# Kernel optimization log

Measured on AMD Instinct MI355X. Metric: run time of the kernel, lower is better.

Reference implementation:

```python
import jax, jax.numpy as jnp
import numpy as np

VAR_EPS = 1e-5
CLAMP = 1e-7
B, S, D = 128, 1024, 256  # D = ambient Lorentz dim (time + D-1 spatial), k = 1


def linner(a, b):
    """Minkowski inner product <a,b>_L = -a0*b0 + sum_i a_i*b_i, keepdims."""
    return -a[..., :1] * b[..., :1] + jnp.sum(a[..., 1:] * b[..., 1:], axis=-1, keepdims=True)


def add_origin(x):
    # x + o where o = (1, 0, ..., 0)
    return jnp.concatenate([x[..., :1] + 1.0, x[..., 1:]], axis=-1)


def centroid(x):
    """Lorentz centroid over dim -2 (k=1): normalize the Euclidean mean back to the hyperboloid."""
    avg = jnp.mean(x, axis=-2)
    denom = jnp.sqrt(jnp.clip(jnp.abs(-linner(avg, avg)), 1e-8, None))
    return avg / denom


def logmap(x, y):
    alpha = jnp.clip(-linner(x, y), 1.0 + CLAMP, None)
    u = y - alpha * x
    return (jnp.arccosh(alpha) / jnp.sqrt(alpha * alpha - 1.0)) * u


def transp0back(x, v):
    # parallel transport from x to origin o: v - v0/(1+x0) * (x+o)
    coef = v[..., :1] / (1.0 + x[..., :1])
    return v - coef * add_origin(x)


def transp0(y, v):
    # parallel transport from origin o to y: v + <y,v>_L/(1+y0) * (o+y)
    coef = linner(y, v) / (1.0 + y[..., :1])
    return v + coef * add_origin(y)


def expmap(x, u):
    n = jnp.sqrt(jnp.clip(linner(u, u), CLAMP, None))
    return jnp.cosh(n) * x + jnp.sinh(n) * (u / n)


def expmap0_space(u_space):
    # exp map at origin from a purely-spatial tangent vector (used only for data generation)
    n = jnp.sqrt(jnp.clip(jnp.sum(u_space * u_space, axis=-1, keepdims=True), CLAMP, None))
    return jnp.concatenate([jnp.cosh(n), jnp.sinh(n) * (u_space / n)], axis=-1)


def setup_inputs() -> dict:
    key = jax.random.key(0)
    k1, = jax.random.split(key, 1)
    u_space = 0.5 * jax.random.normal(k1, (B, S, D - 1), dtype=jnp.float32)
    x = expmap0_space(u_space)  # valid points on the hyperboloid, [B,S,D]
    beta = jnp.zeros((D,), dtype=jnp.float32).at[0].set(1.0)  # manifold.origin
    gamma = jnp.ones((1,), dtype=jnp.float32)
    return {"x": x, "beta": beta, "gamma": gamma}


def reference(x, beta, gamma):
    # training-mode forward of LorentzBatchNorm_beta (3D input path)
    mean = centroid(centroid(x))            # [D] Frechet-style centroid over seq then batch
    x_t = logmap(mean, x)                   # [B,S,D] tangent at mean
    x_t = transp0back(mean, x_t)            # transport to tangent at origin
    var = jnp.sqrt(jnp.var(x_t, axis=(0, 1)) + VAR_EPS)  # [D] per-feature std
    x_t = x_t * (gamma / var)
    x_t = transp0(beta, x_t)                # transport to tangent at beta
    return expmap(beta, x_t)                # [B,S,D] back on the manifold
```

## Files before the change

kernel.cpp:

```cpp
#include <hip/hip_runtime.h>
#include <math.h>

#define BB 128
#define SS 1024
#define DD 256
#define NP (BB * SS)
#define CH 16
#define ROWS (SS / CH)
#define NB3 2048
#define NW3 (NB3 * 4)
#define RB4 32
#define NB4A (NB3 / RB4)

#define LN2F 0.69314718056f
#define L2EF 1.44269504089f
__device__ __forceinline__ float fsqrt(float x) { return __builtin_amdgcn_sqrtf(x); }
__device__ __forceinline__ float frcp(float x)  { return __builtin_amdgcn_rcpf(x); }
__device__ __forceinline__ float frsq(float x)  { return __builtin_amdgcn_rsqf(x); }
__device__ __forceinline__ float flog2(float x) { return __builtin_amdgcn_logf(x); }
__device__ __forceinline__ float fexp2(float x) { return __builtin_amdgcn_exp2f(x); }

__device__ __forceinline__ float wave_sum(float v) {
#pragma unroll
    for (int m = 32; m >= 1; m >>= 1) v += __shfl_xor(v, m, 64);
    return v;
}

__device__ __forceinline__ void wave_sum2(float& a, float& b) {
#pragma unroll
    for (int m = 32; m >= 1; m >>= 1) {
        float ta = __shfl_xor(a, m, 64);
        float tb = __shfl_xor(b, m, 64);
        a += ta;
        b += tb;
    }
}

__device__ __forceinline__ float block_sum(float v, float* red) {
    const int t = threadIdx.x;
    red[t] = v;
    __syncthreads();
#pragma unroll
    for (int off = 128; off >= 1; off >>= 1) {
        if (t < off) red[t] += red[t + off];
        __syncthreads();
    }
    float r = red[0];
    __syncthreads();
    return r;
}

__device__ __forceinline__ float dot4(float4 a, float4 b) {
    return fmaf(a.x, b.x, fmaf(a.y, b.y, fmaf(a.z, b.z, a.w * b.w)));
}

__global__ __launch_bounds__(256) void k1_partial(const float* __restrict__ x,
                                                  float* __restrict__ part) {
    const int ch = blockIdx.x, b = blockIdx.y;
    const int w = threadIdx.x >> 6, l = threadIdx.x & 63;
    const float4* x4 = (const float4*)x;
    size_t base = ((size_t)b * SS + (size_t)ch * ROWS + (size_t)w * (ROWS / 4)) * (DD / 4);
    float4 s = make_float4(0.f, 0.f, 0.f, 0.f);
#pragma unroll 4
    for (int r = 0; r < ROWS / 4; ++r) {
        float4 v = x4[base + (size_t)r * (DD / 4) + l];
        s.x += v.x; s.y += v.y; s.z += v.z; s.w += v.w;
    }
    __shared__ float lds[4][DD];
    lds[w][4 * l + 0] = s.x; lds[w][4 * l + 1] = s.y;
    lds[w][4 * l + 2] = s.z; lds[w][4 * l + 3] = s.w;
    __syncthreads();
    const int t = threadIdx.x;
    part[((size_t)b * CH + ch) * DD + t] = lds[0][t] + lds[1][t] + lds[2][t] + lds[3][t];
}

__global__ __launch_bounds__(256) void k2a_c1(const float* __restrict__ part,
                                              float* __restrict__ c1) {
    const int b = blockIdx.x;
    const int t = threadIdx.x;
    __shared__ float red[DD];
    float sx = 0.f;
#pragma unroll
    for (int ch = 0; ch < CH; ++ch) sx += part[((size_t)b * CH + ch) * DD + t];
    float avg = sx * (1.0f / SS);
    float contrib = (t == 0) ? avg * avg : -avg * avg;
    float r = block_sum(contrib, red);
    c1[(size_t)b * DD + t] = avg * frsq(fmaxf(fabsf(r), 1e-8f));
}

__global__ __launch_bounds__(256) void k2b_mean(const float* __restrict__ c1,
                                                float* __restrict__ wsmean) {
    const int t = threadIdx.x;
    __shared__ float red[DD];
    float acc = 0.f;
#pragma unroll 8
    for (int b = 0; b < BB; ++b) acc += c1[(size_t)b * DD + t];
    float avg = acc * (1.0f / BB);
    float contrib = (t == 0) ? avg * avg : -avg * avg;
    float r = block_sum(contrib, red);
    wsmean[t] = avg * frsq(fmaxf(fabsf(r), 1e-8f));
}

__device__ __forceinline__ float4 compute_xt(const float4* __restrict__ row, int l,
                                             float4 m4, float m0, float inv1pm0) {
    float4 v = row[l];
    float dp = dot4(v, m4);
    float dot = wave_sum(dp);
    float y0 = __shfl(v.x, 0, 64);
    float alpha = fmaxf(fmaf(2.0f * m0, y0, -dot), 1.0f + 1e-7f);
    float tt = fmaf(alpha, alpha, -1.0f);
    float f = (LN2F * flog2(alpha + fsqrt(tt))) * frsq(tt);
    float xt0 = f * (y0 - alpha * m0);
    float coef = xt0 * inv1pm0;
    float4 r;
    r.x = f * (v.x - alpha * m4.x) - coef * ((l == 0) ? (m0 + 1.0f) : m4.x);
    r.y = f * (v.y - alpha * m4.y) - coef * m4.y;
    r.z = f * (v.z - alpha * m4.z) - coef * m4.z;
    r.w = f * (v.w - alpha * m4.w) - coef * m4.w;
    return r;
}

__global__ __launch_bounds__(256, 8) void k3_stats(const float* __restrict__ x,
                                                   const float* __restrict__ wsmean,
                                                   float* __restrict__ part3) {
    const int w = threadIdx.x >> 6, l = threadIdx.x & 63;
    float4 m4 = ((const float4*)wsmean)[l];
    float m0 = wsmean[0];
    float inv1pm0 = frcp(1.0f + m0);
    float4 s = make_float4(0, 0, 0, 0), q = make_float4(0, 0, 0, 0);
    const int wid = blockIdx.x * 4 + w;
#pragma unroll 2
    for (int p = wid; p < NP; p += NW3) {
        const float4* row = ((const float4*)x) + (size_t)p * (DD / 4);
        float4 t4 = compute_xt(row, l, m4, m0, inv1pm0);
        s.x += t4.x; s.y += t4.y; s.z += t4.z; s.w += t4.w;
        q.x += t4.x * t4.x; q.y += t4.y * t4.y; q.z += t4.z * t4.z; q.w += t4.w * t4.w;
    }
    __shared__ float lds[4][2 * DD];
    lds[w][4 * l + 0] = s.x; lds[w][4 * l + 1] = s.y;
    lds[w][4 * l + 2] = s.z; lds[w][4 * l + 3] = s.w;
    lds[w][DD + 4 * l + 0] = q.x; lds[w][DD + 4 * l + 1] = q.y;
    lds[w][DD + 4 * l + 2] = q.z; lds[w][DD + 4 * l + 3] = q.w;
    __syncthreads();
    const int t = threadIdx.x;
    part3[(size_t)blockIdx.x * (2 * DD) + t]      = lds[0][t] + lds[1][t] + lds[2][t] + lds[3][t];
    part3[(size_t)blockIdx.x * (2 * DD) + DD + t] = lds[0][DD + t] + lds[1][DD + t] + lds[2][DD + t] + lds[3][DD + t];
}

__global__ __launch_bounds__(512) void k4a_reduce(const float* __restrict__ part3,
                                                  float* __restrict__ stage2) {
    const int t = threadIdx.x;
    const int r0 = blockIdx.x * RB4;
    float s = 0.f;
#pragma unroll 8
    for (int r = 0; r < RB4; ++r) s += part3[(size_t)(r0 + r) * (2 * DD) + t];
    stage2[(size_t)blockIdx.x * (2 * DD) + t] = s;
}

__global__ __launch_bounds__(256) void k4b_scale(const float* __restrict__ stage2,
                                                 const float* __restrict__ gamma,
                                                 float* __restrict__ wsscale) {
    const int t = threadIdx.x;
    double s1 = 0.0, s2 = 0.0;
    for (int i = 0; i < NB4A; ++i) {
        s1 += (double)stage2[(size_t)i * (2 * DD) + t];
        s2 += (double)stage2[(size_t)i * (2 * DD) + DD + t];
    }
    const double N = (double)NP;
    double mv = s1 / N;
    double var = s2 / N - mv * mv;
    wsscale[t] = gamma[0] * frsq((float)var + 1e-5f);
}

__global__ __launch_bounds__(256, 8) void k5_out(const float* __restrict__ x,
                                                 const float* __restrict__ wsmean,
                                                 const float* __restrict__ wsscale,
                                                 const float* __restrict__ beta,
                                                 float4* __restrict__ out4) {
    const int w = threadIdx.x >> 6, l = threadIdx.x & 63;
    float4 m4 = ((const float4*)wsmean)[l];
    float m0 = wsmean[0];
    float inv1pm0 = frcp(1.0f + m0);
    float4 sc = ((const float4*)wsscale)[l];
    float4 b4 = ((const float4*)beta)[l];
    float b0 = beta[0];
    float inv1pb0 = frcp(1.0f + b0);
    float b0p1 = b0 + 1.0f;
    const int wid = blockIdx.x * 4 + w;
#pragma unroll 2
    for (int p = wid; p < NP; p += NW3) {
        const float4* row = ((const float4*)x) + (size_t)p * (DD / 4);
        float4 t4 = compute_xt(row, l, m4, m0, inv1pm0);
        float4 v = make_float4(t4.x * sc.x, t4.y * sc.y, t4.z * sc.z, t4.w * sc.w);
        float pb = dot4(v, b4);
        float pv = dot4(v, v);
        wave_sum2(pb, pv);
        float v0 = __shfl(v.x, 0, 64);
        float coef = fmaf(-2.0f * b0, v0, pb) * inv1pb0;
        float vvL = fmaf(-2.0f * v0, v0, pv);
        float nn = fmaxf(fmaf(-2.0f * coef, v0, vvL), 1e-7f);
        float n = fsqrt(nn);
        float e = fexp2(n * L2EF);
        float ei = frcp(e);
        float chn = 0.5f * (e + ei);
        float shn = 0.5f * (e - ei) * frsq(nn);
        float4 o;
        o.x = fmaf(chn, (l == 0) ? b0 : b4.x,
                   shn * (v.x + coef * ((l == 0) ? b0p1 : b4.x)));
        o.y = fmaf(chn, b4.y, shn * fmaf(coef, b4.y, v.y));
        o.z = fmaf(chn, b4.z, shn * fmaf(coef, b4.z, v.z));
        o.w = fmaf(chn, b4.w, shn * fmaf(coef, b4.w, v.w));
        out4[(size_t)p * (DD / 4) + l] = o;
    }
}

extern "C" void kernel_launch(void* const* d_in, const int* in_sizes, int n_in,
                              void* d_out, int out_size, void* d_ws, size_t ws_size,
                              hipStream_t stream) {
    (void)in_sizes; (void)n_in; (void)out_size; (void)ws_size;
    const float* x     = (const float*)d_in[0];
    const float* beta  = (const float*)d_in[1];
    const float* gamma = (const float*)d_in[2];
    float* out = (float*)d_out;

    float* wsmean  = (float*)d_ws;
    float* wsscale = wsmean + DD;
    float* scratch = wsscale + DD;

    float* part   = scratch;
    float* c1     = scratch + (size_t)BB * CH * DD;
    float* part3  = scratch;
    float* stage2 = scratch + (size_t)NB3 * 2 * DD;

    k1_partial<<<dim3(CH, BB), 256, 0, stream>>>(x, part);
    k2a_c1<<<BB, 256, 0, stream>>>(part, c1);
    k2b_mean<<<1, 256, 0, stream>>>(c1, wsmean);
    k3_stats<<<NB3, 256, 0, stream>>>(x, wsmean, part3);
    k4a_reduce<<<NB4A, 512, 0, stream>>>(part3, stage2);
    k4b_scale<<<1, 256, 0, stream>>>(stage2, gamma, wsscale);
    k5_out<<<NB3, 256, 0, stream>>>(x, wsmean, wsscale, beta, (float4*)out);
}
```

Measured before the change: 106.2 us.

## Fold single-block mean and scale kernels into per-block prologues of k3 and k5

```diff
diff --git a/kernel.cpp b/kernel.cpp
--- a/kernel.cpp
+++ b/kernel.cpp
@@ -52,6 +52,19 @@
 
 __device__ __forceinline__ float dot4(float4 a, float4 b) {
     return fmaf(a.x, b.x, fmaf(a.y, b.y, fmaf(a.z, b.z, a.w * b.w)));
+}
+
+__device__ __forceinline__ void mean_prologue(const float* __restrict__ c1,
+                                              float* mean_lds, float* red) {
+    const int t = threadIdx.x;
+    float acc = 0.f;
+#pragma unroll 8
+    for (int b = 0; b < BB; ++b) acc += c1[(size_t)b * DD + t];
+    float avg = acc * (1.0f / BB);
+    float contrib = (t == 0) ? avg * avg : -avg * avg;
+    float r = block_sum(contrib, red);
+    mean_lds[t] = avg * frsq(fmaxf(fabsf(r), 1e-8f));
+    __syncthreads();
 }
 
 __global__ __launch_bounds__(256) void k1_partial(const float* __restrict__ x,
@@ -86,19 +99,6 @@
     float contrib = (t == 0) ? avg * avg : -avg * avg;
     float r = block_sum(contrib, red);
     c1[(size_t)b * DD + t] = avg * frsq(fmaxf(fabsf(r), 1e-8f));
-}
-
-__global__ __launch_bounds__(256) void k2b_mean(const float* __restrict__ c1,
-                                                float* __restrict__ wsmean) {
-    const int t = threadIdx.x;
-    __shared__ float red[DD];
-    float acc = 0.f;
-#pragma unroll 8
-    for (int b = 0; b < BB; ++b) acc += c1[(size_t)b * DD + t];
-    float avg = acc * (1.0f / BB);
-    float contrib = (t == 0) ? avg * avg : -avg * avg;
-    float r = block_sum(contrib, red);
-    wsmean[t] = avg * frsq(fmaxf(fabsf(r), 1e-8f));
 }
 
 __device__ __forceinline__ float4 compute_xt(const float4* __restrict__ row, int l,
@@ -121,11 +121,15 @@
 }
 
 __global__ __launch_bounds__(256, 8) void k3_stats(const float* __restrict__ x,
-                                                   const float* __restrict__ wsmean,
+                                                   const float* __restrict__ c1,
                                                    float* __restrict__ part3) {
+    __shared__ float mean_lds[DD];
+    __shared__ float red[DD];
+    mean_prologue(c1, mean_lds, red);
+
     const int w = threadIdx.x >> 6, l = threadIdx.x & 63;
-    float4 m4 = ((const float4*)wsmean)[l];
-    float m0 = wsmean[0];
+    float4 m4 = ((const float4*)mean_lds)[l];
+    float m0 = mean_lds[0];
     float inv1pm0 = frcp(1.0f + m0);
     float4 s = make_float4(0, 0, 0, 0), q = make_float4(0, 0, 0, 0);
     const int wid = blockIdx.x * 4 + w;
@@ -157,31 +161,35 @@
     stage2[(size_t)blockIdx.x * (2 * DD) + t] = s;
 }
 
-__global__ __launch_bounds__(256) void k4b_scale(const float* __restrict__ stage2,
+__global__ __launch_bounds__(256, 8) void k5_out(const float* __restrict__ x,
+                                                 const float* __restrict__ c1,
+                                                 const float* __restrict__ stage2,
                                                  const float* __restrict__ gamma,
-                                                 float* __restrict__ wsscale) {
-    const int t = threadIdx.x;
-    double s1 = 0.0, s2 = 0.0;
-    for (int i = 0; i < NB4A; ++i) {
-        s1 += (double)stage2[(size_t)i * (2 * DD) + t];
-        s2 += (double)stage2[(size_t)i * (2 * DD) + DD + t];
-    }
-    const double N = (double)NP;
-    double mv = s1 / N;
-    double var = s2 / N - mv * mv;
-    wsscale[t] = gamma[0] * frsq((float)var + 1e-5f);
-}
-
-__global__ __launch_bounds__(256, 8) void k5_out(const float* __restrict__ x,
-                                                 const float* __restrict__ wsmean,
-                                                 const float* __restrict__ wsscale,
                                                  const float* __restrict__ beta,
                                                  float4* __restrict__ out4) {
+    __shared__ float mean_lds[DD];
+    __shared__ float scale_lds[DD];
+    __shared__ float red[DD];
+    const int t = threadIdx.x;
+    {
+        double s1 = 0.0, s2 = 0.0;
+#pragma unroll 8
+        for (int i = 0; i < NB4A; ++i) {
+            s1 += (double)stage2[(size_t)i * (2 * DD) + t];
+            s2 += (double)stage2[(size_t)i * (2 * DD) + DD + t];
+        }
+        const double N = (double)NP;
+        double mv = s1 / N;
+        double var = s2 / N - mv * mv;
+        scale_lds[t] = gamma[0] * frsq((float)var + 1e-5f);
+    }
+    mean_prologue(c1, mean_lds, red);
+
     const int w = threadIdx.x >> 6, l = threadIdx.x & 63;
-    float4 m4 = ((const float4*)wsmean)[l];
-    float m0 = wsmean[0];
+    float4 m4 = ((const float4*)mean_lds)[l];
+    float m0 = mean_lds[0];
     float inv1pm0 = frcp(1.0f + m0);
-    float4 sc = ((const float4*)wsscale)[l];
+    float4 sc = ((const float4*)scale_lds)[l];
     float4 b4 = ((const float4*)beta)[l];
     float b0 = beta[0];
     float inv1pb0 = frcp(1.0f + b0);
@@ -223,20 +231,15 @@
     const float* gamma = (const float*)d_in[2];
     float* out = (float*)d_out;
 
-    float* wsmean  = (float*)d_ws;
-    float* wsscale = wsmean + DD;
-    float* scratch = wsscale + DD;
-
-    float* part   = scratch;
-    float* c1     = scratch + (size_t)BB * CH * DD;
-    float* part3  = scratch;
-    float* stage2 = scratch + (size_t)NB3 * 2 * DD;
+    float* scratch = (float*)d_ws;
+    float* c1     = scratch;
+    float* part   = scratch + 32768;
+    float* part3  = scratch + 32768;
+    float* stage2 = scratch + 32768 + 1048576;
 
     k1_partial<<<dim3(CH, BB), 256, 0, stream>>>(x, part);
     k2a_c1<<<BB, 256, 0, stream>>>(part, c1);
-    k2b_mean<<<1, 256, 0, stream>>>(c1, wsmean);
-    k3_stats<<<NB3, 256, 0, stream>>>(x, wsmean, part3);
+    k3_stats<<<NB3, 256, 0, stream>>>(x, c1, part3);
     k4a_reduce<<<NB4A, 512, 0, stream>>>(part3, stage2);
-    k4b_scale<<<1, 256, 0, stream>>>(stage2, gamma, wsscale);
-    k5_out<<<NB3, 256, 0, stream>>>(x, wsmean, wsscale, beta, (float4*)out);
-}
+    k5_out<<<NB3, 256, 0, stream>>>(x, c1, stage2, gamma, beta, (float4*)out);
+}
```

After: 119.0 us. 1.12x slower.
